# Optimization experiments

Measured on AMD Instinct MI355X. Metric: run time of the kernel, lower is better.

## Reference

```python
import jax, jax.numpy as jnp
import numpy as np


def _quantize(m):
    # per-row symmetric int8 quantization: absmax over last dim, round to nearest-even
    max_val = jnp.max(jnp.abs(m), axis=-1)          # [...]
    q = jnp.round(m * (127.0 / max_val)[..., None])  # values in [-127, 127], kept in fp32
    return q, max_val


def setup_inputs() -> dict:
    key = jax.random.key(0)
    k1, k2, k3 = jax.random.split(key, 3)
    B, S, D_IN, D_OUT = 4, 8192, 1024, 1024
    x = jax.random.normal(k1, (B, S, D_IN), dtype=jnp.float32)
    weight = jax.random.normal(k2, (D_OUT, D_IN), dtype=jnp.float32) * 0.02
    bias = jax.random.normal(k3, (D_OUT,), dtype=jnp.float32)
    return {"x": x, "weight": weight, "bias": bias}


def reference(x, weight, bias):
    # weight quantization happens once in __init__; replicated here for self-containment
    w_q, w_max = _quantize(weight)    # [N,K], [N]
    x_q, x_max = _quantize(x)         # [B,S,K], [B,S]
    # int8 GEMM emulated in fp32, exactly as the original module does
    res_q = jnp.einsum('bsk,nk->bsn', x_q, w_q)            # [B,S,N] fp32
    mx = x_max[..., None] * w_max                          # outer-product dequant scale [B,S,N]
    res = (res_q / (127.0 * 127.0)).astype(jnp.float16) * mx  # fp16 * fp32 -> fp32
    return res + bias
```

## Files before the change

kernel.cpp:

```cpp
#include <hip/hip_runtime.h>
#include <hip/hip_fp16.h>


typedef int i32x4 __attribute__((ext_vector_type(4)));

#define BM 256
#define BN 256
#define BKB 64

__global__ __launch_bounds__(256) void quant_rows_kernel(
    const float* __restrict__ in, signed char* __restrict__ q,
    float* __restrict__ rowmax, int K) {
  const int row = blockIdx.x;
  const int t = threadIdx.x;
  const size_t base = (size_t)row * K;
  float4 v = reinterpret_cast<const float4*>(in + base)[t];
  float a = fmaxf(fmaxf(fabsf(v.x), fabsf(v.y)), fmaxf(fabsf(v.z), fabsf(v.w)));
#pragma unroll
  for (int off = 32; off > 0; off >>= 1) a = fmaxf(a, __shfl_xor(a, off, 64));
  __shared__ float smax[4];
  if ((t & 63) == 0) smax[t >> 6] = a;
  __syncthreads();
  float m = fmaxf(fmaxf(smax[0], smax[1]), fmaxf(smax[2], smax[3]));
  float s = 127.0f / m;
  char4 qq;
  qq.x = (signed char)(int)rintf(v.x * s);
  qq.y = (signed char)(int)rintf(v.y * s);
  qq.z = (signed char)(int)rintf(v.z * s);
  qq.w = (signed char)(int)rintf(v.w * s);
  reinterpret_cast<char4*>(q + base)[t] = qq;
  if (t == 0) rowmax[row] = m;
}

__device__ __forceinline__ void gload_lds16(const void* g, void* l) {
  __builtin_amdgcn_global_load_lds(
      (const __attribute__((address_space(1))) unsigned char*)g,
      (__attribute__((address_space(3))) unsigned char*)l, 16, 0, 0);
}

__global__ __launch_bounds__(512, 2) void w8x8_gemm_kernel(
    const signed char* __restrict__ Aq, const signed char* __restrict__ Bq,
    const float* __restrict__ Amax, const float* __restrict__ Bmax,
    const float* __restrict__ bias, float* __restrict__ out,
    int M, int N, int K, int cpx) {
  __shared__ __align__(16) signed char ldsA[3 * BM * BKB];
  __shared__ __align__(16) signed char ldsB[3 * BN * BKB];
  const int t = threadIdx.x;
  const int lane = t & 63;
  const int wave = t >> 6;
  const int wm = wave >> 2;
  const int wn = wave & 3;

  const int nbn = N / BN;
  const int bid = blockIdx.x;
  const int tile = (bid & 7) * cpx + (bid >> 3);
  const int bm = tile / nbn, bn = tile % nbn;

  const signed char* Abase = Aq + (size_t)bm * BM * K;
  const signed char* Bbase = Bq + (size_t)bn * BN * K;

  const int rS = t >> 2;
  const int lcS = (t & 3) ^ ((rS >> 1) & 3);
  const size_t gA0 = (size_t)rS * K + lcS * 16;
  const size_t gA1 = gA0 + (size_t)128 * K;
  const int dd0 = t * 16, dd1 = t * 16 + 8192;

  const int fr = lane & 15, fq = lane >> 4;
  const int pc = fq ^ ((fr >> 1) & 3);
  const int aoff0 = (wm * 128 + fr) * BKB + pc * 16;
  const int boff0 = (wn * 64 + fr) * BKB + pc * 16;

  i32x4 acc[8][4];
#pragma unroll
  for (int m = 0; m < 8; ++m)
#pragma unroll
    for (int n = 0; n < 4; ++n) acc[m][n] = (i32x4){0, 0, 0, 0};

#define STAGE_A(bf, kt)                                                     \
  do {                                                                      \
    gload_lds16(Abase + gA0 + (size_t)(kt) * BKB, ldsA + (bf)*16384 + dd0); \
    gload_lds16(Abase + gA1 + (size_t)(kt) * BKB, ldsA + (bf)*16384 + dd1); \
  } while (0)
#define STAGE_B(bf, kt)                                                     \
  do {                                                                      \
    gload_lds16(Bbase + gA0 + (size_t)(kt) * BKB, ldsB + (bf)*16384 + dd0); \
    gload_lds16(Bbase + gA1 + (size_t)(kt) * BKB, ldsB + (bf)*16384 + dd1); \
  } while (0)

  const int NT = K / BKB;
  STAGE_A(0, 0);
  STAGE_B(0, 0);
  STAGE_A(1, 1);
  STAGE_B(1, 1);
  asm volatile("s_waitcnt vmcnt(4)" ::: "memory");
  __builtin_amdgcn_s_barrier();

  int cb = 0;
  for (int kt = 0; kt < NT; ++kt) {
    const signed char* lA = ldsA + cb * 16384;
    const signed char* lB = ldsB + cb * 16384;
    int sb = cb + 2;
    if (sb >= 3) sb -= 3;
    const bool pf = (kt + 2 < NT);

    i32x4 a[8], b[4];
#pragma unroll
    for (int m = 0; m < 8; ++m)
      a[m] = *reinterpret_cast<const i32x4*>(lA + aoff0 + m * (16 * BKB));
    b[0] = *reinterpret_cast<const i32x4*>(lB + boff0);
    b[1] = *reinterpret_cast<const i32x4*>(lB + boff0 + 16 * BKB);
    if (pf) STAGE_A(sb, kt + 2);
    __builtin_amdgcn_s_barrier();
    __builtin_amdgcn_s_setprio(1);
#pragma unroll
    for (int m = 0; m < 8; ++m) {
      acc[m][0] =
          __builtin_amdgcn_mfma_i32_16x16x64_i8(a[m], b[0], acc[m][0], 0, 0, 0);
      acc[m][1] =
          __builtin_amdgcn_mfma_i32_16x16x64_i8(a[m], b[1], acc[m][1], 0, 0, 0);
    }
    __builtin_amdgcn_s_setprio(0);
    __builtin_amdgcn_s_barrier();

    b[2] = *reinterpret_cast<const i32x4*>(lB + boff0 + 2 * 16 * BKB);
    b[3] = *reinterpret_cast<const i32x4*>(lB + boff0 + 3 * 16 * BKB);
    if (pf) STAGE_B(sb, kt + 2);
    __builtin_amdgcn_s_barrier();
    __builtin_amdgcn_s_setprio(1);
#pragma unroll
    for (int m = 0; m < 8; ++m) {
      acc[m][2] =
          __builtin_amdgcn_mfma_i32_16x16x64_i8(a[m], b[2], acc[m][2], 0, 0, 0);
      acc[m][3] =
          __builtin_amdgcn_mfma_i32_16x16x64_i8(a[m], b[3], acc[m][3], 0, 0, 0);
    }
    __builtin_amdgcn_s_setprio(0);
    if (pf)
      asm volatile("s_waitcnt vmcnt(4)" ::: "memory");
    else
      asm volatile("s_waitcnt vmcnt(0)" ::: "memory");
    __builtin_amdgcn_s_barrier();
    cb = (cb + 1 == 3) ? 0 : cb + 1;
  }
#undef STAGE_A
#undef STAGE_B

  const int row0 = bm * BM + wm * 128;
  const int col0 = bn * BN + wn * 64;
#pragma unroll
  for (int n = 0; n < 4; ++n) {
    int col = col0 + n * 16 + fr;
    float wmx = Bmax[col];
    float bs = bias[col];
#pragma unroll
    for (int m = 0; m < 8; ++m) {
      int rowq = row0 + m * 16 + fq * 4;
#pragma unroll
      for (int r = 0; r < 4; ++r) {
        int row = rowq + r;
        float xm = Amax[row];
        float v = (float)acc[m][n][r] / 16129.0f;
        float h = __half2float(__float2half_rn(v));
        out[(size_t)row * N + col] = h * (xm * wmx) + bs;
      }
    }
  }
}

extern "C" void kernel_launch(void* const* d_in, const int* in_sizes, int n_in,
                              void* d_out, int out_size, void* d_ws, size_t ws_size,
                              hipStream_t stream) {
  const float* x = (const float*)d_in[0];
  const float* w = (const float*)d_in[1];
  const float* bias = (const float*)d_in[2];
  float* out = (float*)d_out;

  const int N = in_sizes[2];
  const int K = in_sizes[1] / N;
  const int M = in_sizes[0] / K;

  signed char* xq = (signed char*)d_ws;
  signed char* wq = xq + (size_t)M * K;
  float* xmax = (float*)(wq + (size_t)N * K);
  float* wmax = xmax + M;

  quant_rows_kernel<<<M, 256, 0, stream>>>(x, xq, xmax, K);
  quant_rows_kernel<<<N, 256, 0, stream>>>(w, wq, wmax, K);

  const int nwg = (M / BM) * (N / BN);
  const int cpx = nwg / 8;
  w8x8_gemm_kernel<<<nwg, 512, 0, stream>>>(xq, wq, xmax, wmax, bias, out,
                                            M, N, K, cpx);
}
```

Measured before the change: 107.8 us.

## Switch GEMM to double-buffered LDS with single MFMA phase and higher occupancy bound

Replaces the three-stage LDS ring with a two-buffer ping-pong: the next K-tile's A and B are both loaded at the top of each iteration, and all 32 MFMAs run in one phase with one barrier. This removes the split A/B staging and several extra barriers per iteration. The launch bound minimum-blocks hint rises from 2 to 4, and the epilogue is reordered row-major and multiplies by a reciprocal instead of dividing. The risks: a 4-blocks-per-CU bound squeezes registers far below what the 128-register accumulator needs and may cause spills, and a shallower prefetch hides less load latency.

```diff
diff --git a/kernel.cpp b/kernel.cpp
--- a/kernel.cpp
+++ b/kernel.cpp
@@ -38,13 +38,13 @@
       (__attribute__((address_space(3))) unsigned char*)l, 16, 0, 0);
 }
 
-__global__ __launch_bounds__(512, 2) void w8x8_gemm_kernel(
+__global__ __launch_bounds__(512, 4) void w8x8_gemm_kernel(
     const signed char* __restrict__ Aq, const signed char* __restrict__ Bq,
     const float* __restrict__ Amax, const float* __restrict__ Bmax,
     const float* __restrict__ bias, float* __restrict__ out,
     int M, int N, int K, int cpx) {
-  __shared__ __align__(16) signed char ldsA[3 * BM * BKB];
-  __shared__ __align__(16) signed char ldsB[3 * BN * BKB];
+  __shared__ __align__(16) signed char ldsA[2 * BM * BKB];
+  __shared__ __align__(16) signed char ldsB[2 * BN * BKB];
   const int t = threadIdx.x;
   const int lane = t & 63;
   const int wave = t >> 6;
@@ -76,92 +76,70 @@
 #pragma unroll
     for (int n = 0; n < 4; ++n) acc[m][n] = (i32x4){0, 0, 0, 0};
 
-#define STAGE_A(bf, kt)                                                     \
+#define STAGE(bf, kt)                                                       \
   do {                                                                      \
     gload_lds16(Abase + gA0 + (size_t)(kt) * BKB, ldsA + (bf)*16384 + dd0); \
     gload_lds16(Abase + gA1 + (size_t)(kt) * BKB, ldsA + (bf)*16384 + dd1); \
-  } while (0)
-#define STAGE_B(bf, kt)                                                     \
-  do {                                                                      \
     gload_lds16(Bbase + gA0 + (size_t)(kt) * BKB, ldsB + (bf)*16384 + dd0); \
     gload_lds16(Bbase + gA1 + (size_t)(kt) * BKB, ldsB + (bf)*16384 + dd1); \
   } while (0)
 
   const int NT = K / BKB;
-  STAGE_A(0, 0);
-  STAGE_B(0, 0);
-  STAGE_A(1, 1);
-  STAGE_B(1, 1);
-  asm volatile("s_waitcnt vmcnt(4)" ::: "memory");
+  STAGE(0, 0);
+  asm volatile("s_waitcnt vmcnt(0)" ::: "memory");
   __builtin_amdgcn_s_barrier();
 
-  int cb = 0;
   for (int kt = 0; kt < NT; ++kt) {
-    const signed char* lA = ldsA + cb * 16384;
-    const signed char* lB = ldsB + cb * 16384;
-    int sb = cb + 2;
-    if (sb >= 3) sb -= 3;
-    const bool pf = (kt + 2 < NT);
+    const signed char* lA = ldsA + (kt & 1) * 16384;
+    const signed char* lB = ldsB + (kt & 1) * 16384;
+    const bool pf = (kt + 1 < NT);
+    if (pf) STAGE((kt + 1) & 1, kt + 1);
 
     i32x4 a[8], b[4];
 #pragma unroll
     for (int m = 0; m < 8; ++m)
       a[m] = *reinterpret_cast<const i32x4*>(lA + aoff0 + m * (16 * BKB));
-    b[0] = *reinterpret_cast<const i32x4*>(lB + boff0);
-    b[1] = *reinterpret_cast<const i32x4*>(lB + boff0 + 16 * BKB);
-    if (pf) STAGE_A(sb, kt + 2);
-    __builtin_amdgcn_s_barrier();
+#pragma unroll
+    for (int n = 0; n < 4; ++n)
+      b[n] = *reinterpret_cast<const i32x4*>(lB + boff0 + n * (16 * BKB));
     __builtin_amdgcn_s_setprio(1);
 #pragma unroll
-    for (int m = 0; m < 8; ++m) {
-      acc[m][0] =
-          __builtin_amdgcn_mfma_i32_16x16x64_i8(a[m], b[0], acc[m][0], 0, 0, 0);
-      acc[m][1] =
-          __builtin_amdgcn_mfma_i32_16x16x64_i8(a[m], b[1], acc[m][1], 0, 0, 0);
+    for (int m = 0; m < 8; ++m)
+#pragma unroll
+      for (int n = 0; n < 4; ++n)
+        acc[m][n] = __builtin_amdgcn_mfma_i32_16x16x64_i8(a[m], b[n],
+                                                          acc[m][n], 0, 0, 0);
+    __builtin_amdgcn_s_setprio(0);
+
+    if (pf) {
+      asm volatile("s_waitcnt vmcnt(0)" ::: "memory");
+      __builtin_amdgcn_s_barrier();
     }
-    __builtin_amdgcn_s_setprio(0);
-    __builtin_amdgcn_s_barrier();
-
-    b[2] = *reinterpret_cast<const i32x4*>(lB + boff0 + 2 * 16 * BKB);
-    b[3] = *reinterpret_cast<const i32x4*>(lB + boff0 + 3 * 16 * BKB);
-    if (pf) STAGE_B(sb, kt + 2);
-    __builtin_amdgcn_s_barrier();
-    __builtin_amdgcn_s_setprio(1);
-#pragma unroll
-    for (int m = 0; m < 8; ++m) {
-      acc[m][2] =
-          __builtin_amdgcn_mfma_i32_16x16x64_i8(a[m], b[2], acc[m][2], 0, 0, 0);
-      acc[m][3] =
-          __builtin_amdgcn_mfma_i32_16x16x64_i8(a[m], b[3], acc[m][3], 0, 0, 0);
-    }
-    __builtin_amdgcn_s_setprio(0);
-    if (pf)
-      asm volatile("s_waitcnt vmcnt(4)" ::: "memory");
-    else
-      asm volatile("s_waitcnt vmcnt(0)" ::: "memory");
-    __builtin_amdgcn_s_barrier();
-    cb = (cb + 1 == 3) ? 0 : cb + 1;
   }
-#undef STAGE_A
-#undef STAGE_B
+#undef STAGE
 
   const int row0 = bm * BM + wm * 128;
   const int col0 = bn * BN + wn * 64;
+  const float C = 1.0f / 16129.0f;
+  float wmx[4], bs[4];
 #pragma unroll
   for (int n = 0; n < 4; ++n) {
     int col = col0 + n * 16 + fr;
-    float wmx = Bmax[col];
-    float bs = bias[col];
+    wmx[n] = Bmax[col];
+    bs[n] = bias[col];
+  }
 #pragma unroll
-    for (int m = 0; m < 8; ++m) {
-      int rowq = row0 + m * 16 + fq * 4;
+  for (int m = 0; m < 8; ++m) {
 #pragma unroll
-      for (int r = 0; r < 4; ++r) {
-        int row = rowq + r;
-        float xm = Amax[row];
-        float v = (float)acc[m][n][r] / 16129.0f;
+    for (int r = 0; r < 4; ++r) {
+      int row = row0 + m * 16 + fq * 4 + r;
+      float xm = Amax[row];
+      float* orow = out + (size_t)row * N;
+#pragma unroll
+      for (int n = 0; n < 4; ++n) {
+        float v = (float)acc[m][n][r] * C;
         float h = __half2float(__float2half_rn(v));
-        out[(size_t)row * N + col] = h * (xm * wmx) + bs;
+        orow[col0 + n * 16 + fr] = h * (xm * wmx[n]) + bs[n];
       }
     }
   }
```

New measurement: 397.6 us. 269% more time.
